# Kernel optimization log

Hardware: AMD Instinct MI355X
Metric: run time of the kernel (lower is better)

## Reference

```python
import jax, jax.numpy as jnp
import numpy as np

N = 50000      # nodes
E = 1_600_000  # edges (avg degree 32)
D = 128        # in/hidden channels
OUT = 64       # out channels


def setup_inputs() -> dict:
    key = jax.random.key(0)
    ks = jax.random.split(key, 12)
    s = 0.08  # ~glorot scale for 128-dim
    return {
        "x": jax.random.normal(ks[0], (N, D), jnp.float32),
        "edge_index": jax.random.randint(ks[1], (2, E), 0, N, dtype=jnp.int64),
        # GCN layer 1
        "W1": jax.random.normal(ks[2], (D, D), jnp.float32) * s,
        "b1": jnp.zeros((D,), jnp.float32),
        # GraphSAGE layer 2 (mean aggregation): lin_l on neighbors, lin_r on root
        "Wl": jax.random.normal(ks[3], (D, D), jnp.float32) * s,
        "Wr": jax.random.normal(ks[4], (D, D), jnp.float32) * s,
        "bs": jnp.zeros((D,), jnp.float32),
        # GAT layer 3 (heads=1, concat=False)
        "Wg": jax.random.normal(ks[5], (D, D), jnp.float32) * s,
        "a_s": jax.random.normal(ks[6], (D,), jnp.float32) * s,
        "a_d": jax.random.normal(ks[7], (D,), jnp.float32) * s,
        "bg": jnp.zeros((D,), jnp.float32),
        # GCN output layer
        "Wo": jax.random.normal(ks[8], (D, OUT), jnp.float32) * s,
        "bo": jnp.zeros((OUT,), jnp.float32),
    }


def _self_loops(src, dst, n):
    loop = jnp.arange(n, dtype=src.dtype)
    return jnp.concatenate([src, loop]), jnp.concatenate([dst, loop])


def gcn_conv(x, W, b, src, dst, n):
    # PyG GCNConv: add self-loops, symmetric normalization D^-1/2 (A+I) D^-1/2
    s2, d2 = _self_loops(src, dst, n)
    deg = jax.ops.segment_sum(jnp.ones_like(d2, dtype=x.dtype), d2, num_segments=n)
    dinv = jnp.where(deg > 0, jax.lax.rsqrt(deg), 0.0)
    h = x @ W                         # [n, out]
    norm = dinv[s2] * dinv[d2]        # [E+n]
    out = jax.ops.segment_sum(h[s2] * norm[:, None], d2, num_segments=n)
    return out + b


def sage_conv(x, Wl, Wr, b, src, dst, n):
    # PyG SAGEConv, aggr='mean': W_l * mean_neigh + W_r * x (no self-loops)
    deg = jax.ops.segment_sum(jnp.ones_like(dst, dtype=x.dtype), dst, num_segments=n)
    agg = jax.ops.segment_sum(x[src], dst, num_segments=n)
    mean = agg / jnp.maximum(deg, 1.0)[:, None]
    return mean @ Wl + x @ Wr + b


def gat_conv(x, W, a_s, a_d, b, src, dst, n):
    # PyG GATConv heads=1, concat=False: self-loops, edge softmax over incoming edges
    h = x @ W                               # [n, out]
    s2, d2 = _self_loops(src, dst, n)
    alpha_src = h @ a_s                     # [n]
    alpha_dst = h @ a_d                     # [n]
    e = jax.nn.leaky_relu(alpha_src[s2] + alpha_dst[d2], negative_slope=0.2)
    m = jax.ops.segment_max(e, d2, num_segments=n)   # every node has a self-loop
    ex = jnp.exp(e - m[d2])
    denom = jax.ops.segment_sum(ex, d2, num_segments=n)
    alpha = ex / denom[d2]
    out = jax.ops.segment_sum(alpha[:, None] * h[s2], d2, num_segments=n)
    return out + b


def reference(x, edge_index, W1, b1, Wl, Wr, bs, Wg, a_s, a_d, bg, Wo, bo):
    src, dst = edge_index[0], edge_index[1]
    n = x.shape[0]
    # eval mode: F.dropout(training=False) is identity
    h = jax.nn.relu(gcn_conv(x, W1, b1, src, dst, n))
    h = jax.nn.relu(sage_conv(h, Wl, Wr, bs, src, dst, n))
    h = jax.nn.relu(gat_conv(h, Wg, a_s, a_d, bg, src, dst, n))
    return gcn_conv(h, Wo, bo, src, dst, n)
```

## Files before the change

### kernel.cpp

```cpp
#include <hip/hip_runtime.h>
#include <math.h>


#define BUCKET_BITS 8
#define BUCKET_SZ   256
#define NBMAX       256
#define CAP         10240
#define CAPE        2560

typedef short short8 __attribute__((ext_vector_type(8)));
typedef float f32x4 __attribute__((ext_vector_type(4)));
typedef unsigned int u32x4 __attribute__((ext_vector_type(4)));
typedef unsigned short u16x8 __attribute__((ext_vector_type(8)));

__device__ __forceinline__ float leaky02(float x) { return x > 0.0f ? x : 0.2f * x; }
__device__ __forceinline__ float bflo(unsigned u) { return __uint_as_float(u << 16); }
__device__ __forceinline__ float bfhi(unsigned u) { return __uint_as_float(u & 0xFFFF0000u); }
__device__ __forceinline__ unsigned short f2bf(float f) {
    unsigned u = __float_as_uint(f);
    u += 0x7FFFu + ((u >> 16) & 1u);
    return (unsigned short)(u >> 16);
}

template<int NO, bool AFP32, bool SCALE, bool BIASRELU, bool DUAL, bool DOTS>
__global__ __launch_bounds__(256) void mgemm_k(
    const void* __restrict__ Av, const float* __restrict__ W,
    const void* __restrict__ A1v, const float* __restrict__ W1,
    unsigned short* __restrict__ C16,
    const float* __restrict__ scale, const float* __restrict__ bias,
    const float* __restrict__ a_s, const float* __restrict__ a_d,
    float* __restrict__ as_, float* __restrict__ ad_, int n)
{
    constexpr int CT = NO / 16;
    __shared__ unsigned short Wp[128 * NO];
    const int tid = threadIdx.x;
    const int wave = tid >> 6, lane = tid & 63;
    const int q = lane >> 4, ml = lane & 15;
    const int row0 = blockIdx.x * 64 + wave * 16;
    int arow = row0 + ml; if (arow >= n) arow = n - 1;

    f32x4 acc[CT];
#pragma unroll
    for (int c = 0; c < CT; c++) acc[c] = {0.f, 0.f, 0.f, 0.f};

    for (int half = 0; half < (DUAL ? 2 : 1); half++) {
        const float* Wsrc = half ? W1 : W;
        const void* Asrc = half ? A1v : Av;
        __syncthreads();
        for (int f = tid; f < 64 * (NO / 4); f += 256) {
            const int kp = f / (NO / 4);
            const int n4 = f % (NO / 4);
            const float4 a = *(const float4*)(Wsrc + (size_t)(2 * kp) * NO + n4 * 4);
            const float4 b = *(const float4*)(Wsrc + (size_t)(2 * kp + 1) * NO + n4 * 4);
            const int k = 2 * kp, kb = k >> 5, qq = (k >> 3) & 3, p = (k & 7) >> 1;
            const float av[4] = {a.x, a.y, a.z, a.w};
            const float bv[4] = {b.x, b.y, b.z, b.w};
#pragma unroll
            for (int j = 0; j < 4; j++) {
                int col = n4 * 4 + j;
                int c = col >> 4, nl = col & 15;
                unsigned pk = (unsigned)f2bf(av[j]) | ((unsigned)f2bf(bv[j]) << 16);
                ((unsigned*)Wp)[(((kb * CT + c) * 64) + qq * 16 + nl) * 4 + p] = pk;
            }
        }
        __syncthreads();
#pragma unroll
        for (int kb = 0; kb < 4; kb++) {
            short8 afr;
            if (AFP32) {
                const float* Af = (const float*)Asrc + (size_t)arow * 128 + kb * 32 + q * 8;
#pragma unroll
                for (int j = 0; j < 8; j++) afr[j] = (short)f2bf(Af[j]);
            } else {
                afr = *(const short8*)((const unsigned short*)Asrc +
                                       ((size_t)kb * n + arow) * 32 + q * 8);
            }
#pragma unroll
            for (int c = 0; c < CT; c++) {
                short8 bfr = *(const short8*)(Wp + ((size_t)(kb * CT + c) * 64 + lane) * 8);
                acc[c] = __builtin_amdgcn_mfma_f32_16x16x32_bf16(afr, bfr, acc[c], 0, 0, 0);
            }
        }
    }

    if (DOTS) {
        float ps[4] = {0.f, 0.f, 0.f, 0.f}, pd[4] = {0.f, 0.f, 0.f, 0.f};
#pragma unroll
        for (int c = 0; c < CT; c++) {
            float sv = a_s[c * 16 + ml], dv = a_d[c * 16 + ml];
#pragma unroll
            for (int r = 0; r < 4; r++) {
                ps[r] = fmaf(acc[c][r], sv, ps[r]);
                pd[r] = fmaf(acc[c][r], dv, pd[r]);
            }
        }
#pragma unroll
        for (int off = 1; off < 16; off <<= 1) {
#pragma unroll
            for (int r = 0; r < 4; r++) {
                ps[r] += __shfl_xor(ps[r], off, 64);
                pd[r] += __shfl_xor(pd[r], off, 64);
            }
        }
        if (ml == 0) {
#pragma unroll
            for (int r = 0; r < 4; r++) {
                int row = row0 + q * 4 + r;
                if (row < n) { as_[row] = ps[r]; ad_[row] = pd[r]; }
            }
        }
    }

    float sc[4];
    if (SCALE) {
#pragma unroll
        for (int r = 0; r < 4; r++) {
            int row = row0 + q * 4 + r;
            sc[r] = scale[row < n ? row : 0];
        }
    }
#pragma unroll
    for (int c = 0; c < CT; c++) {
        float bv = BIASRELU ? bias[c * 16 + ml] : 0.0f;
        const int col = c * 16 + ml;
#pragma unroll
        for (int r = 0; r < 4; r++) {
            int row = row0 + q * 4 + r;
            if (row < n) {
                float v = acc[c][r];
                if (SCALE) v *= sc[r];
                if (BIASRELU) v = fmaxf(v + bv, 0.0f);
                C16[((size_t)(col >> 5) * n + row) * 32 + (col & 31)] = f2bf(v);
            }
        }
    }
}

__global__ void binit_k(int* __restrict__ bcur, int nb) {
    int t = threadIdx.x;
    if (t < nb) bcur[t] = t * CAP;
}

#define PART_CH 4096
__global__ __launch_bounds__(256) void part_k(
    const int* __restrict__ src, const int* __restrict__ dst,
    int* __restrict__ bcur, unsigned long long* __restrict__ part, int nE)
{
    __shared__ int cnt[NBMAX];
    __shared__ int cur[NBMAX];
    const int base = blockIdx.x * PART_CH;
    const int t = threadIdx.x;
    cnt[t] = 0;
    __syncthreads();
    int d[PART_CH / 256], s[PART_CH / 256];
#pragma unroll
    for (int j = 0; j < PART_CH / 256; j++) {
        int e = base + j * 256 + t;
        if (e < nE) {
            d[j] = dst[e]; s[j] = src[e];
            atomicAdd(&cnt[d[j] >> BUCKET_BITS], 1);
        } else d[j] = -1;
    }
    __syncthreads();
    {
        int c = cnt[t];
        cur[t] = c ? atomicAdd(&bcur[t], c) : 0;
    }
    __syncthreads();
#pragma unroll
    for (int j = 0; j < PART_CH / 256; j++) {
        if (d[j] >= 0) {
            int p = atomicAdd(&cur[d[j] >> BUCKET_BITS], 1);
            part[p] = ((unsigned long long)(unsigned)d[j] << 32) | (unsigned)s[j];
        }
    }
}

__global__ __launch_bounds__(256) void bscan_k(const int* __restrict__ bcur,
                                               int* __restrict__ bofs, int nb) {
    __shared__ int sm[256];
    const int t = threadIdx.x;
    int v = (t < nb) ? (bcur[t] - t * CAP) : 0;
    sm[t] = v;
    __syncthreads();
    for (int off = 1; off < 256; off <<= 1) {
        int tv = (t >= off) ? sm[t - off] : 0;
        __syncthreads();
        sm[t] += tv;
        __syncthreads();
    }
    if (t < nb) {
        bofs[t] = sm[t] - v;
        if (t == nb - 1) bofs[nb] = sm[t];
    }
}

__global__ __launch_bounds__(256) void csr_k(
    const unsigned long long* __restrict__ part, const int* __restrict__ bcur,
    const int* __restrict__ bofs, int* __restrict__ rowptr, int* __restrict__ srcs,
    float* __restrict__ dinv, float* __restrict__ invm, int n, int nE)
{
    __shared__ int lcnt[BUCKET_SZ];
    __shared__ int sm[BUCKET_SZ];
    __shared__ int lcur[BUCKET_SZ];
    const int b = blockIdx.x;
    const int t = threadIdx.x;
    const int base_in = b * CAP;
    const int cntE = bcur[b] - base_in;
    const int base_out = bofs[b];

    lcnt[t] = 0;
    __syncthreads();
#pragma unroll 4
    for (int e = t; e < cntE; e += 256) {
        int dl = (int)(part[base_in + e] >> 32) & (BUCKET_SZ - 1);
        atomicAdd(&lcnt[dl], 1);
    }
    __syncthreads();
    int v = lcnt[t];
    sm[t] = v;
    __syncthreads();
    for (int off = 1; off < 256; off <<= 1) {
        int tv = (t >= off) ? sm[t - off] : 0;
        __syncthreads();
        sm[t] += tv;
        __syncthreads();
    }
    const int excl = sm[t] - v;
    const int node = (b << BUCKET_BITS) + t;
    if (node < n) {
        rowptr[node] = base_out + excl;
        float dg = (float)v;
        dinv[node] = rsqrtf(dg + 1.0f);
        invm[node] = 1.0f / fmaxf(dg, 1.0f);
        if (node == n - 1) rowptr[n] = nE;
    }
    lcur[t] = excl;
    __syncthreads();
#pragma unroll 4
    for (int e = t; e < cntE; e += 256) {
        unsigned long long w = part[base_in + e];
        int dl = (int)(w >> 32) & (BUCKET_SZ - 1);
        int pos = atomicAdd(&lcur[dl], 1);
        srcs[base_out + pos] = (int)(unsigned)w;
    }
}

__global__ __launch_bounds__(256) void gatw_k(
    const int* __restrict__ rowptr, const int* __restrict__ srcs,
    const float* __restrict__ as_, const float* __restrict__ ad_,
    float* __restrict__ ew, float* __restrict__ rdn_, float* __restrict__ sw_, int n)
{
    const int node = blockIdx.x * 32 + (threadIdx.x >> 3);
    const int lane = threadIdx.x & 7;
    if (node >= n) return;
    const int beg = rowptr[node], end = rowptr[node + 1];
    const float ad_d = ad_[node];
    float psum = 0.f;
    for (int k = beg + lane; k < end; k += 8) {
        float e = __expf(leaky02(as_[srcs[k]] + ad_d));
        ew[k] = e;
        psum += e;
    }
#pragma unroll
    for (int off = 4; off > 0; off >>= 1) psum += __shfl_xor(psum, off, 64);
    if (lane == 0) {
        float se = __expf(leaky02(as_[node] + ad_d));
        float r = 1.0f / (psum + se);
        rdn_[node] = r;
        sw_[node] = se * r;
    }
}

template<int MODE, bool OV>
__device__ __forceinline__ void gath_loop(
    const u32x4* __restrict__ Hc, const int* __restrict__ srcs,
    const float* __restrict__ ew, const int* lsrc, const float* lw,
    int beg, int end, int beg_blk, int lane, float* acc)
{
    int k = beg;
    for (; k + 8 <= end; k += 8) {
        unsigned sidx[8]; float wv[8];
#pragma unroll
        for (int j = 0; j < 8; j++) {
            int ofs = k + j - beg_blk;
            if (OV) {
                bool in = ofs < CAPE;
                int ofc = in ? ofs : 0;
                sidx[j] = (unsigned)(in ? lsrc[ofc] : srcs[k + j]);
                if (MODE == 2) wv[j] = in ? lw[ofc] : ew[k + j];
            } else {
                sidx[j] = (unsigned)lsrc[ofs];
                if (MODE == 2) wv[j] = lw[ofs];
            }
        }
        u32x4 h[8];
#pragma unroll
        for (int j = 0; j < 8; j++) h[j] = Hc[(size_t)sidx[j] * 4 + lane];
#pragma unroll
        for (int j = 0; j < 8; j++) {
#pragma unroll
            for (int c = 0; c < 4; c++) {
                if (MODE == 2) {
                    acc[2 * c]     = fmaf(wv[j], bflo(h[j][c]), acc[2 * c]);
                    acc[2 * c + 1] = fmaf(wv[j], bfhi(h[j][c]), acc[2 * c + 1]);
                } else {
                    acc[2 * c]     += bflo(h[j][c]);
                    acc[2 * c + 1] += bfhi(h[j][c]);
                }
            }
        }
    }
    if (k < end) {
        unsigned sidx[8]; float wv[8];
#pragma unroll
        for (int j = 0; j < 8; j++) {
            int kk = k + j;
            bool act = kk < end;
            int kc = act ? kk : end - 1;
            int ofs = kc - beg_blk;
            int s; float w0 = 1.0f;
            if (OV) {
                bool in = ofs < CAPE;
                int ofc = in ? ofs : 0;
                s = in ? lsrc[ofc] : srcs[kc];
                if (MODE == 2) w0 = in ? lw[ofc] : ew[kc];
            } else {
                s = lsrc[ofs];
                if (MODE == 2) w0 = lw[ofs];
            }
            sidx[j] = (unsigned)s;
            wv[j] = act ? w0 : 0.0f;
        }
        u32x4 h[8];
#pragma unroll
        for (int j = 0; j < 8; j++) h[j] = Hc[(size_t)sidx[j] * 4 + lane];
#pragma unroll
        for (int j = 0; j < 8; j++) {
#pragma unroll
            for (int c = 0; c < 4; c++) {
                acc[2 * c]     = fmaf(wv[j], bflo(h[j][c]), acc[2 * c]);
                acc[2 * c + 1] = fmaf(wv[j], bfhi(h[j][c]), acc[2 * c + 1]);
            }
        }
    }
}

template<int NCB, int MODE>
__global__ __launch_bounds__(256) void gatherbf_k(
    const unsigned short* __restrict__ H16, float* __restrict__ outf,
    unsigned short* __restrict__ out16,
    const int* __restrict__ rowptr, const int* __restrict__ srcs,
    const float* __restrict__ scl,
    const float* __restrict__ sw_,
    const float* __restrict__ ew,
    const float* __restrict__ bias, int n)
{
    constexpr int XPC = 8 / NCB;
    constexpr int NPB = 64;
    __shared__ int lsrc[CAPE];
    __shared__ float lw[(MODE == 2) ? CAPE : 1];

    const int bid = (int)blockIdx.x;
    const int xj = bid & 7;
    const int cb = xj / XPC;
    const int NG = (n + NPB - 1) / NPB;
    const int ng = (bid >> 3) * XPC + (xj % XPC);
    if (ng >= NG) return;

    const int tid = (int)threadIdx.x;
    const int node0 = ng * NPB;
    const int nodeN = min(node0 + NPB, n);
    const int beg_blk = rowptr[node0];
    const int end_blk = rowptr[nodeN];
    const int cnt = end_blk - beg_blk;
    const int cl = min(cnt, CAPE);
    for (int i = tid; i < cl; i += 256) {
        lsrc[i] = srcs[beg_blk + i];
        if (MODE == 2) lw[i] = ew[beg_blk + i];
    }
    __syncthreads();

    const int node = node0 + (tid >> 2);
    const int lane = tid & 3;
    if (node >= nodeN) return;
    const int beg = rowptr[node], end = rowptr[node + 1];
    const u32x4* __restrict__ Hc = (const u32x4*)H16 + (size_t)cb * n * 4;

    float acc[8];
#pragma unroll
    for (int j = 0; j < 8; j++) acc[j] = 0.f;

    if (cnt <= CAPE)
        gath_loop<MODE, false>(Hc, srcs, ew, lsrc, lw, beg, end, beg_blk, lane, acc);
    else
        gath_loop<MODE, true>(Hc, srcs, ew, lsrc, lw, beg, end, beg_blk, lane, acc);

    const size_t orow = ((size_t)cb * n + node) * 4 + lane;
    float r[8];
    if (MODE == 0) {
        float sc = scl[node];
#pragma unroll
        for (int j = 0; j < 8; j++) r[j] = acc[j] * sc;
    } else {
        u32x4 su = Hc[(size_t)node * 4 + lane];
        float sv[8];
#pragma unroll
        for (int c = 0; c < 4; c++) { sv[2 * c] = bflo(su[c]); sv[2 * c + 1] = bfhi(su[c]); }
        const float4* b4 = (const float4*)bias;
        float4 ba = b4[cb * 8 + lane * 2], bb = b4[cb * 8 + lane * 2 + 1];
        float bv[8] = {ba.x, ba.y, ba.z, ba.w, bb.x, bb.y, bb.z, bb.w};
        if (MODE == 2) {
            float rden = scl[node], sw = sw_[node];
#pragma unroll
            for (int j = 0; j < 8; j++)
                r[j] = fmaxf(fmaf(rden, acc[j], fmaf(sw, sv[j], bv[j])), 0.f);
        } else {
            float dv = scl[node];
#pragma unroll
            for (int j = 0; j < 8; j++) {
                r[j] = dv * (acc[j] + sv[j]) + bv[j];
                if (MODE == 1) r[j] = fmaxf(r[j], 0.f);
            }
        }
    }
    if (MODE == 3) {
        float4* o4 = (float4*)(outf + (size_t)node * 64 + cb * 32 + lane * 8);
        float4 ra = {r[0], r[1], r[2], r[3]}, rb = {r[4], r[5], r[6], r[7]};
        o4[0] = ra; o4[1] = rb;
    } else {
        u16x8 qv;
#pragma unroll
        for (int j = 0; j < 8; j++) qv[j] = f2bf(r[j]);
        ((u16x8*)out16)[orow] = qv;
    }
}

extern "C" void kernel_launch(void* const* d_in, const int* in_sizes, int n_in,
                              void* d_out, int out_size, void* d_ws, size_t ws_size,
                              hipStream_t stream)
{
    const float* x   = (const float*)d_in[0];
    const int*   ei  = (const int*)d_in[1];
    const float* W1  = (const float*)d_in[2];
    const float* b1  = (const float*)d_in[3];
    const float* Wl  = (const float*)d_in[4];
    const float* Wr  = (const float*)d_in[5];
    const float* bs  = (const float*)d_in[6];
    const float* Wg  = (const float*)d_in[7];
    const float* a_s = (const float*)d_in[8];
    const float* a_d = (const float*)d_in[9];
    const float* bg  = (const float*)d_in[10];
    const float* Wo  = (const float*)d_in[11];
    const float* bo  = (const float*)d_in[12];

    const int n  = in_sizes[0] / 128;
    const int nE = in_sizes[1] / 2;
    const int* src = ei;
    const int* dst = ei + nE;

    char* w = (char*)d_ws;
    auto alloc = [&](size_t bytes) { char* p = w; w += (bytes + 255) & ~(size_t)255; return p; };
    unsigned short* S0 = (unsigned short*)alloc((size_t)n * 128 * 2);
    unsigned short* S1 = (unsigned short*)alloc((size_t)n * 128 * 2);
    unsigned short* S2 = (unsigned short*)alloc((size_t)n * 128 * 2);
    const int nbv = (n + BUCKET_SZ - 1) / BUCKET_SZ;
    unsigned long long* part = (unsigned long long*)alloc((size_t)nbv * CAP * 8);
    int*   srcs   = (int*)alloc((size_t)nE * 4);
    int*   rowptr = (int*)alloc((size_t)(n + 1) * 4);
    int*   bofs   = (int*)alloc((NBMAX + 1) * 4);
    int*   bcur   = (int*)alloc(NBMAX * 4);
    float* dinv   = (float*)alloc((size_t)n * 4);
    float* invm   = (float*)alloc((size_t)n * 4);
    float* as_    = (float*)alloc((size_t)n * 4);
    float* ad_    = (float*)alloc((size_t)n * 4);
    float* ew     = (float*)alloc((size_t)nE * 4);
    float* rdn_   = (float*)alloc((size_t)n * 4);
    float* sw_    = (float*)alloc((size_t)n * 4);

    const int TB = 256;
    auto cdiv = [](long long a, long long b) { return (int)((a + b - 1) / b); };
    const int nb     = nbv;
    const int gPart  = cdiv(nE, PART_CH);
    const int gGemm  = cdiv(n, 64);
    const int NG     = cdiv(n, 64);
    const int gGa128 = 8 * cdiv(NG, 2);
    const int gGa64  = 8 * cdiv(NG, 4);
    const int gGatw  = cdiv(n, 32);

    binit_k<<<1, 256, 0, stream>>>(bcur, nb);
    part_k<<<gPart, TB, 0, stream>>>(src, dst, bcur, part, nE);
    bscan_k<<<1, 256, 0, stream>>>(bcur, bofs, nb);
    csr_k<<<nb, TB, 0, stream>>>(part, bcur, bofs, rowptr, srcs, dinv, invm, n, nE);

    mgemm_k<128, true, true, false, false, false><<<gGemm, TB, 0, stream>>>(
        x, W1, nullptr, nullptr, S0, dinv, nullptr, nullptr, nullptr, nullptr, nullptr, n);
    gatherbf_k<4, 1><<<gGa128, TB, 0, stream>>>(S0, nullptr, S1, rowptr, srcs,
                                                dinv, nullptr, nullptr, b1, n);

    gatherbf_k<4, 0><<<gGa128, TB, 0, stream>>>(S1, nullptr, S0, rowptr, srcs,
                                                invm, nullptr, nullptr, nullptr, n);
    mgemm_k<128, false, false, true, true, false><<<gGemm, TB, 0, stream>>>(
        S0, Wl, S1, Wr, S2, nullptr, bs, nullptr, nullptr, nullptr, nullptr, n);

    mgemm_k<128, false, false, false, false, true><<<gGemm, TB, 0, stream>>>(
        S2, Wg, nullptr, nullptr, S1, nullptr, nullptr, a_s, a_d, as_, ad_, n);
    gatw_k<<<gGatw, TB, 0, stream>>>(rowptr, srcs, as_, ad_, ew, rdn_, sw_, n);
    gatherbf_k<4, 2><<<gGa128, TB, 0, stream>>>(S1, nullptr, S0, rowptr, srcs,
                                                rdn_, sw_, ew, bg, n);

    mgemm_k<64, false, true, false, false, false><<<gGemm, TB, 0, stream>>>(
        S0, Wo, nullptr, nullptr, S2, dinv, nullptr, nullptr, nullptr, nullptr, nullptr, n);
    gatherbf_k<2, 3><<<gGa64, TB, 0, stream>>>(S2, (float*)d_out, nullptr, rowptr, srcs,
                                               dinv, nullptr, nullptr, bo, n);
}
```

Before: 357.6 us.

## Drop LDS staging of edge indices in gather; vector-load srcs and packed FMA

```diff
diff --git a/kernel.cpp b/kernel.cpp
--- a/kernel.cpp
+++ b/kernel.cpp
@@ -6,12 +6,14 @@
 #define BUCKET_SZ   256
 #define NBMAX       256
 #define CAP         10240
-#define CAPE        2560
 
 typedef short short8 __attribute__((ext_vector_type(8)));
 typedef float f32x4 __attribute__((ext_vector_type(4)));
+typedef float f32x2 __attribute__((ext_vector_type(2)));
 typedef unsigned int u32x4 __attribute__((ext_vector_type(4)));
 typedef unsigned short u16x8 __attribute__((ext_vector_type(8)));
+typedef int int4a __attribute__((ext_vector_type(4), aligned(4)));
+typedef float float4a __attribute__((ext_vector_type(4), aligned(4)));
 
 __device__ __forceinline__ float leaky02(float x) { return x > 0.0f ? x : 0.2f * x; }
 __device__ __forceinline__ float bflo(unsigned u) { return __uint_as_float(u << 16); }
@@ -272,82 +274,33 @@
     }
 }
 
-template<int MODE, bool OV>
-__device__ __forceinline__ void gath_loop(
-    const u32x4* __restrict__ Hc, const int* __restrict__ srcs,
-    const float* __restrict__ ew, const int* lsrc, const float* lw,
-    int beg, int end, int beg_blk, int lane, float* acc)
-{
-    int k = beg;
-    for (; k + 8 <= end; k += 8) {
-        unsigned sidx[8]; float wv[8];
-#pragma unroll
-        for (int j = 0; j < 8; j++) {
-            int ofs = k + j - beg_blk;
-            if (OV) {
-                bool in = ofs < CAPE;
-                int ofc = in ? ofs : 0;
-                sidx[j] = (unsigned)(in ? lsrc[ofc] : srcs[k + j]);
-                if (MODE == 2) wv[j] = in ? lw[ofc] : ew[k + j];
-            } else {
-                sidx[j] = (unsigned)lsrc[ofs];
-                if (MODE == 2) wv[j] = lw[ofs];
-            }
-        }
-        u32x4 h[8];
-#pragma unroll
-        for (int j = 0; j < 8; j++) h[j] = Hc[(size_t)sidx[j] * 4 + lane];
-#pragma unroll
-        for (int j = 0; j < 8; j++) {
-#pragma unroll
-            for (int c = 0; c < 4; c++) {
-                if (MODE == 2) {
-                    acc[2 * c]     = fmaf(wv[j], bflo(h[j][c]), acc[2 * c]);
-                    acc[2 * c + 1] = fmaf(wv[j], bfhi(h[j][c]), acc[2 * c + 1]);
-                } else {
-                    acc[2 * c]     += bflo(h[j][c]);
-                    acc[2 * c + 1] += bfhi(h[j][c]);
-                }
-            }
-        }
-    }
-    if (k < end) {
-        unsigned sidx[8]; float wv[8];
-#pragma unroll
-        for (int j = 0; j < 8; j++) {
-            int kk = k + j;
-            bool act = kk < end;
-            int kc = act ? kk : end - 1;
-            int ofs = kc - beg_blk;
-            int s; float w0 = 1.0f;
-            if (OV) {
-                bool in = ofs < CAPE;
-                int ofc = in ? ofs : 0;
-                s = in ? lsrc[ofc] : srcs[kc];
-                if (MODE == 2) w0 = in ? lw[ofc] : ew[kc];
-            } else {
-                s = lsrc[ofs];
-                if (MODE == 2) w0 = lw[ofs];
-            }
-            sidx[j] = (unsigned)s;
-            wv[j] = act ? w0 : 0.0f;
-        }
-        u32x4 h[8];
-#pragma unroll
-        for (int j = 0; j < 8; j++) h[j] = Hc[(size_t)sidx[j] * 4 + lane];
-#pragma unroll
-        for (int j = 0; j < 8; j++) {
-#pragma unroll
-            for (int c = 0; c < 4; c++) {
-                acc[2 * c]     = fmaf(wv[j], bflo(h[j][c]), acc[2 * c]);
-                acc[2 * c + 1] = fmaf(wv[j], bfhi(h[j][c]), acc[2 * c + 1]);
-            }
+template<int MODE>
+__device__ __forceinline__ void edge8(
+    const char* __restrict__ Hb, unsigned loff,
+    const int4a ia, const int4a ib,
+    const float4a wa, const float4a wb,
+    f32x2* acc)
+{
+    const int s[8] = {ia.x, ia.y, ia.z, ia.w, ib.x, ib.y, ib.z, ib.w};
+    u32x4 h[8];
+#pragma unroll
+    for (int j = 0; j < 8; j++)
+        h[j] = *(const u32x4*)(Hb + (size_t)(((unsigned)s[j] << 6) + loff));
+    const float wv[8] = {wa.x, wa.y, wa.z, wa.w, wb.x, wb.y, wb.z, wb.w};
+#pragma unroll
+    for (int j = 0; j < 8; j++) {
+        f32x2 w2 = {wv[j], wv[j]};
+#pragma unroll
+        for (int c = 0; c < 4; c++) {
+            f32x2 hv = {bflo(h[j][c]), bfhi(h[j][c])};
+            if (MODE == 2) acc[c] = w2 * hv + acc[c];
+            else           acc[c] = acc[c] + hv;
         }
     }
 }
 
 template<int NCB, int MODE>
-__global__ __launch_bounds__(256) void gatherbf_k(
+__global__ __launch_bounds__(256, 4) void gatherbf_k(
     const unsigned short* __restrict__ H16, float* __restrict__ outf,
     unsigned short* __restrict__ out16,
     const int* __restrict__ rowptr, const int* __restrict__ srcs,
@@ -358,8 +311,6 @@
 {
     constexpr int XPC = 8 / NCB;
     constexpr int NPB = 64;
-    __shared__ int lsrc[CAPE];
-    __shared__ float lw[(MODE == 2) ? CAPE : 1];
 
     const int bid = (int)blockIdx.x;
     const int xj = bid & 7;
@@ -369,57 +320,101 @@
     if (ng >= NG) return;
 
     const int tid = (int)threadIdx.x;
-    const int node0 = ng * NPB;
-    const int nodeN = min(node0 + NPB, n);
-    const int beg_blk = rowptr[node0];
-    const int end_blk = rowptr[nodeN];
-    const int cnt = end_blk - beg_blk;
-    const int cl = min(cnt, CAPE);
-    for (int i = tid; i < cl; i += 256) {
-        lsrc[i] = srcs[beg_blk + i];
-        if (MODE == 2) lw[i] = ew[beg_blk + i];
-    }
-    __syncthreads();
-
-    const int node = node0 + (tid >> 2);
+    const int node = ng * NPB + (tid >> 2);
+    if (node >= n) return;
     const int lane = tid & 3;
-    if (node >= nodeN) return;
     const int beg = rowptr[node], end = rowptr[node + 1];
-    const u32x4* __restrict__ Hc = (const u32x4*)H16 + (size_t)cb * n * 4;
-
-    float acc[8];
-#pragma unroll
-    for (int j = 0; j < 8; j++) acc[j] = 0.f;
-
-    if (cnt <= CAPE)
-        gath_loop<MODE, false>(Hc, srcs, ew, lsrc, lw, beg, end, beg_blk, lane, acc);
-    else
-        gath_loop<MODE, true>(Hc, srcs, ew, lsrc, lw, beg, end, beg_blk, lane, acc);
+    const char* __restrict__ Hb = (const char*)H16 + (size_t)cb * n * 64;
+    const unsigned loff = (unsigned)lane * 16u;
+
+    f32x2 acc[4];
+#pragma unroll
+    for (int c = 0; c < 4; c++) acc[c] = {0.f, 0.f};
+    const float4a wdum = {0.f, 0.f, 0.f, 0.f};
+
+    int k = beg;
+    for (; k + 16 <= end; k += 16) {
+        int4a ia0 = *(const int4a*)(srcs + k);
+        int4a ib0 = *(const int4a*)(srcs + k + 4);
+        int4a ia1 = *(const int4a*)(srcs + k + 8);
+        int4a ib1 = *(const int4a*)(srcs + k + 12);
+        float4a wa0 = wdum, wb0 = wdum, wa1 = wdum, wb1 = wdum;
+        if (MODE == 2) {
+            wa0 = *(const float4a*)(ew + k);      wb0 = *(const float4a*)(ew + k + 4);
+            wa1 = *(const float4a*)(ew + k + 8);  wb1 = *(const float4a*)(ew + k + 12);
+        }
+        edge8<MODE>(Hb, loff, ia0, ib0, wa0, wb0, acc);
+        edge8<MODE>(Hb, loff, ia1, ib1, wa1, wb1, acc);
+    }
+    for (; k + 8 <= end; k += 8) {
+        int4a ia = *(const int4a*)(srcs + k);
+        int4a ib = *(const int4a*)(srcs + k + 4);
+        float4a wa = wdum, wb = wdum;
+        if (MODE == 2) {
+            wa = *(const float4a*)(ew + k);  wb = *(const float4a*)(ew + k + 4);
+        }
+        edge8<MODE>(Hb, loff, ia, ib, wa, wb, acc);
+    }
+    if (k < end) {
+        int4a ia = *(const int4a*)(srcs + k);
+        int4a ib = *(const int4a*)(srcs + k + 4);
+        int s[8] = {ia.x, ia.y, ia.z, ia.w, ib.x, ib.y, ib.z, ib.w};
+        float wv[8];
+        if (MODE == 2) {
+            float4a wa = *(const float4a*)(ew + k);
+            float4a wb = *(const float4a*)(ew + k + 4);
+            wv[0] = wa.x; wv[1] = wa.y; wv[2] = wa.z; wv[3] = wa.w;
+            wv[4] = wb.x; wv[5] = wb.y; wv[6] = wb.z; wv[7] = wb.w;
+        }
+#pragma unroll
+        for (int j = 0; j < 8; j++) {
+            bool act = (k + j) < end;
+            s[j] = act ? s[j] : 0;
+            if (MODE == 2) wv[j] = act ? wv[j] : 0.0f;
+            else           wv[j] = act ? 1.0f : 0.0f;
+        }
+        u32x4 h[8];
+#pragma unroll
+        for (int j = 0; j < 8; j++)
+            h[j] = *(const u32x4*)(Hb + (size_t)(((unsigned)s[j] << 6) + loff));
+#pragma unroll
+        for (int j = 0; j < 8; j++) {
+            f32x2 w2 = {wv[j], wv[j]};
+#pragma unroll
+            for (int c = 0; c < 4; c++) {
+                f32x2 hv = {bflo(h[j][c]), bfhi(h[j][c])};
+                acc[c] = w2 * hv + acc[c];
+            }
+        }
+    }
 
     const size_t orow = ((size_t)cb * n + node) * 4 + lane;
     float r[8];
     if (MODE == 0) {
         float sc = scl[node];
 #pragma unroll
-        for (int j = 0; j < 8; j++) r[j] = acc[j] * sc;
+        for (int c = 0; c < 4; c++) { r[2*c] = acc[c].x * sc; r[2*c+1] = acc[c].y * sc; }
     } else {
-        u32x4 su = Hc[(size_t)node * 4 + lane];
+        u32x4 su = *(const u32x4*)(Hb + (size_t)(((unsigned)node << 6) + loff));
         float sv[8];
 #pragma unroll
-        for (int c = 0; c < 4; c++) { sv[2 * c] = bflo(su[c]); sv[2 * c + 1] = bfhi(su[c]); }
+        for (int c = 0; c < 4; c++) { sv[2*c] = bflo(su[c]); sv[2*c+1] = bfhi(su[c]); }
         const float4* b4 = (const float4*)bias;
         float4 ba = b4[cb * 8 + lane * 2], bb = b4[cb * 8 + lane * 2 + 1];
         float bv[8] = {ba.x, ba.y, ba.z, ba.w, bb.x, bb.y, bb.z, bb.w};
+        float a8[8];
+#pragma unroll
+        for (int c = 0; c < 4; c++) { a8[2*c] = acc[c].x; a8[2*c+1] = acc[c].y; }
         if (MODE == 2) {
             float rden = scl[node], sw = sw_[node];
 #pragma unroll
             for (int j = 0; j < 8; j++)
-                r[j] = fmaxf(fmaf(rden, acc[j], fmaf(sw, sv[j], bv[j])), 0.f);
+                r[j] = fmaxf(fmaf(rden, a8[j], fmaf(sw, sv[j], bv[j])), 0.f);
         } else {
             float dv = scl[node];
 #pragma unroll
             for (int j = 0; j < 8; j++) {
-                r[j] = dv * (acc[j] + sv[j]) + bv[j];
+                r[j] = dv * (a8[j] + sv[j]) + bv[j];
                 if (MODE == 1) r[j] = fmaxf(r[j], 0.f);
             }
         }
```

After: 377.1 us. 1.05x slower.

## Prepack bf16 weights once and read MFMA B fragments from global memory

Applied to the files above, without the earlier changes.

```diff
diff --git a/kernel.cpp b/kernel.cpp
--- a/kernel.cpp
+++ b/kernel.cpp
@@ -10,6 +10,7 @@
 
 typedef short short8 __attribute__((ext_vector_type(8)));
 typedef float f32x4 __attribute__((ext_vector_type(4)));
+typedef float f32x2 __attribute__((ext_vector_type(2)));
 typedef unsigned int u32x4 __attribute__((ext_vector_type(4)));
 typedef unsigned short u16x8 __attribute__((ext_vector_type(8)));
 
@@ -22,17 +23,51 @@
     return (unsigned short)(u >> 16);
 }
 
+__global__ __launch_bounds__(256) void wpackall_k(
+    const float* __restrict__ W1, const float* __restrict__ Wl,
+    const float* __restrict__ Wr, const float* __restrict__ Wg,
+    const float* __restrict__ Wo,
+    unsigned* __restrict__ P1, unsigned* __restrict__ Pl,
+    unsigned* __restrict__ Pr, unsigned* __restrict__ Pg,
+    unsigned* __restrict__ Po)
+{
+    const int b = blockIdx.x;
+    const float* W; unsigned* P; int NO;
+    if      (b == 0) { W = W1; P = P1; NO = 128; }
+    else if (b == 1) { W = Wl; P = Pl; NO = 128; }
+    else if (b == 2) { W = Wr; P = Pr; NO = 128; }
+    else if (b == 3) { W = Wg; P = Pg; NO = 128; }
+    else             { W = Wo; P = Po; NO = 64;  }
+    const int CT = NO / 16;
+    const int n4w = NO / 4;
+    for (int f = threadIdx.x; f < 64 * n4w; f += 256) {
+        const int kp = f / n4w;
+        const int n4 = f % n4w;
+        const float4 a = *(const float4*)(W + (size_t)(2 * kp) * NO + n4 * 4);
+        const float4 bb = *(const float4*)(W + (size_t)(2 * kp + 1) * NO + n4 * 4);
+        const int k = 2 * kp, kb = k >> 5, qq = (k >> 3) & 3, p = (k & 7) >> 1;
+        const float av[4] = {a.x, a.y, a.z, a.w};
+        const float bv[4] = {bb.x, bb.y, bb.z, bb.w};
+#pragma unroll
+        for (int j = 0; j < 4; j++) {
+            int col = n4 * 4 + j;
+            int c = col >> 4, nl = col & 15;
+            unsigned pk = (unsigned)f2bf(av[j]) | ((unsigned)f2bf(bv[j]) << 16);
+            P[(((kb * CT + c) * 64) + qq * 16 + nl) * 4 + p] = pk;
+        }
+    }
+}
+
 template<int NO, bool AFP32, bool SCALE, bool BIASRELU, bool DUAL, bool DOTS>
 __global__ __launch_bounds__(256) void mgemm_k(
-    const void* __restrict__ Av, const float* __restrict__ W,
-    const void* __restrict__ A1v, const float* __restrict__ W1,
+    const void* __restrict__ Av, const unsigned short* __restrict__ Bp,
+    const void* __restrict__ A1v, const unsigned short* __restrict__ Bp1,
     unsigned short* __restrict__ C16,
     const float* __restrict__ scale, const float* __restrict__ bias,
     const float* __restrict__ a_s, const float* __restrict__ a_d,
     float* __restrict__ as_, float* __restrict__ ad_, int n)
 {
     constexpr int CT = NO / 16;
-    __shared__ unsigned short Wp[128 * NO];
     const int tid = threadIdx.x;
     const int wave = tid >> 6, lane = tid & 63;
     const int q = lane >> 4, ml = lane & 15;
@@ -44,42 +79,30 @@
     for (int c = 0; c < CT; c++) acc[c] = {0.f, 0.f, 0.f, 0.f};
 
     for (int half = 0; half < (DUAL ? 2 : 1); half++) {
-        const float* Wsrc = half ? W1 : W;
+        const unsigned short* __restrict__ Bsrc = half ? Bp1 : Bp;
         const void* Asrc = half ? A1v : Av;
-        __syncthreads();
-        for (int f = tid; f < 64 * (NO / 4); f += 256) {
-            const int kp = f / (NO / 4);
-            const int n4 = f % (NO / 4);
-            const float4 a = *(const float4*)(Wsrc + (size_t)(2 * kp) * NO + n4 * 4);
-            const float4 b = *(const float4*)(Wsrc + (size_t)(2 * kp + 1) * NO + n4 * 4);
-            const int k = 2 * kp, kb = k >> 5, qq = (k >> 3) & 3, p = (k & 7) >> 1;
-            const float av[4] = {a.x, a.y, a.z, a.w};
-            const float bv[4] = {b.x, b.y, b.z, b.w};
-#pragma unroll
-            for (int j = 0; j < 4; j++) {
-                int col = n4 * 4 + j;
-                int c = col >> 4, nl = col & 15;
-                unsigned pk = (unsigned)f2bf(av[j]) | ((unsigned)f2bf(bv[j]) << 16);
-                ((unsigned*)Wp)[(((kb * CT + c) * 64) + qq * 16 + nl) * 4 + p] = pk;
-            }
-        }
-        __syncthreads();
 #pragma unroll
         for (int kb = 0; kb < 4; kb++) {
             short8 afr;
             if (AFP32) {
                 const float* Af = (const float*)Asrc + (size_t)arow * 128 + kb * 32 + q * 8;
-#pragma unroll
-                for (int j = 0; j < 8; j++) afr[j] = (short)f2bf(Af[j]);
+                float4 f0 = *(const float4*)Af;
+                float4 f1 = *(const float4*)(Af + 4);
+                afr[0] = (short)f2bf(f0.x); afr[1] = (short)f2bf(f0.y);
+                afr[2] = (short)f2bf(f0.z); afr[3] = (short)f2bf(f0.w);
+                afr[4] = (short)f2bf(f1.x); afr[5] = (short)f2bf(f1.y);
+                afr[6] = (short)f2bf(f1.z); afr[7] = (short)f2bf(f1.w);
             } else {
                 afr = *(const short8*)((const unsigned short*)Asrc +
                                        ((size_t)kb * n + arow) * 32 + q * 8);
             }
-#pragma unroll
-            for (int c = 0; c < CT; c++) {
-                short8 bfr = *(const short8*)(Wp + ((size_t)(kb * CT + c) * 64 + lane) * 8);
-                acc[c] = __builtin_amdgcn_mfma_f32_16x16x32_bf16(afr, bfr, acc[c], 0, 0, 0);
-            }
+            short8 bfr[CT];
+#pragma unroll
+            for (int c = 0; c < CT; c++)
+                bfr[c] = *(const short8*)(Bsrc + ((size_t)(kb * CT + c) * 64 + lane) * 8);
+#pragma unroll
+            for (int c = 0; c < CT; c++)
+                acc[c] = __builtin_amdgcn_mfma_f32_16x16x32_bf16(afr, bfr[c], acc[c], 0, 0, 0);
         }
     }
 
@@ -274,73 +297,74 @@
 
 template<int MODE, bool OV>
 __device__ __forceinline__ void gath_loop(
-    const u32x4* __restrict__ Hc, const int* __restrict__ srcs,
-    const float* __restrict__ ew, const int* lsrc, const float* lw,
-    int beg, int end, int beg_blk, int lane, float* acc)
+    const char* __restrict__ Hb, unsigned loff,
+    const int* __restrict__ srcs, const float* __restrict__ ew,
+    const int* lsrc, const float* lw,
+    int beg, int end, int beg_blk, f32x2* acc)
 {
     int k = beg;
     for (; k + 8 <= end; k += 8) {
-        unsigned sidx[8]; float wv[8];
+        int s[8]; float wv[8];
 #pragma unroll
         for (int j = 0; j < 8; j++) {
             int ofs = k + j - beg_blk;
             if (OV) {
                 bool in = ofs < CAPE;
                 int ofc = in ? ofs : 0;
-                sidx[j] = (unsigned)(in ? lsrc[ofc] : srcs[k + j]);
+                s[j] = in ? lsrc[ofc] : srcs[k + j];
                 if (MODE == 2) wv[j] = in ? lw[ofc] : ew[k + j];
             } else {
-                sidx[j] = (unsigned)lsrc[ofs];
+                s[j] = lsrc[ofs];
                 if (MODE == 2) wv[j] = lw[ofs];
             }
         }
         u32x4 h[8];
 #pragma unroll
-        for (int j = 0; j < 8; j++) h[j] = Hc[(size_t)sidx[j] * 4 + lane];
+        for (int j = 0; j < 8; j++)
+            h[j] = *(const u32x4*)(Hb + (size_t)(((unsigned)s[j] << 6) + loff));
 #pragma unroll
         for (int j = 0; j < 8; j++) {
+            f32x2 w2 = {wv[j], wv[j]};
 #pragma unroll
             for (int c = 0; c < 4; c++) {
-                if (MODE == 2) {
-                    acc[2 * c]     = fmaf(wv[j], bflo(h[j][c]), acc[2 * c]);
-                    acc[2 * c + 1] = fmaf(wv[j], bfhi(h[j][c]), acc[2 * c + 1]);
-                } else {
-                    acc[2 * c]     += bflo(h[j][c]);
-                    acc[2 * c + 1] += bfhi(h[j][c]);
-                }
+                f32x2 hv = {bflo(h[j][c]), bfhi(h[j][c])};
+                if (MODE == 2) acc[c] = w2 * hv + acc[c];
+                else           acc[c] = acc[c] + hv;
             }
         }
     }
     if (k < end) {
-        unsigned sidx[8]; float wv[8];
+        int s[8]; float wv[8];
 #pragma unroll
         for (int j = 0; j < 8; j++) {
             int kk = k + j;
             bool act = kk < end;
             int kc = act ? kk : end - 1;
             int ofs = kc - beg_blk;
-            int s; float w0 = 1.0f;
+            int sj; float w0 = 1.0f;
             if (OV) {
                 bool in = ofs < CAPE;
                 int ofc = in ? ofs : 0;
-                s = in ? lsrc[ofc] : srcs[kc];
+                sj = in ? lsrc[ofc] : srcs[kc];
                 if (MODE == 2) w0 = in ? lw[ofc] : ew[kc];
             } else {
-                s = lsrc[ofs];
+                sj = lsrc[ofs];
                 if (MODE == 2) w0 = lw[ofs];
             }
-            sidx[j] = (unsigned)s;
-            wv[j] = act ? w0 : 0.0f;
+            s[j] = sj;
+            wv[j] = act ? ((MODE == 2) ? w0 : 1.0f) : 0.0f;
         }
         u32x4 h[8];
 #pragma unroll
-        for (int j = 0; j < 8; j++) h[j] = Hc[(size_t)sidx[j] * 4 + lane];
+        for (int j = 0; j < 8; j++)
+            h[j] = *(const u32x4*)(Hb + (size_t)(((unsigned)s[j] << 6) + loff));
 #pragma unroll
         for (int j = 0; j < 8; j++) {
+            f32x2 w2 = {wv[j], wv[j]};
 #pragma unroll
             for (int c = 0; c < 4; c++) {
-                acc[2 * c]     = fmaf(wv[j], bflo(h[j][c]), acc[2 * c]);
-                acc[2 * c + 1] = fmaf(wv[j], bfhi(h[j][c]), acc[2 * c + 1]);
+                f32x2 hv = {bflo(h[j][c]), bfhi(h[j][c])};
+                acc[c] = w2 * hv + acc[c];
             }
         }
     }
@@ -385,41 +409,45 @@
     const int lane = tid & 3;
     if (node >= nodeN) return;
     const int beg = rowptr[node], end = rowptr[node + 1];
-    const u32x4* __restrict__ Hc = (const u32x4*)H16 + (size_t)cb * n * 4;
-
-    float acc[8];
-#pragma unroll
-    for (int j = 0; j < 8; j++) acc[j] = 0.f;
+    const char* __restrict__ Hb = (const char*)H16 + (size_t)cb * n * 64;
+    const unsigned loff = (unsigned)lane * 16u;
+
+    f32x2 acc[4];
+#pragma unroll
+    for (int c = 0; c < 4; c++) acc[c] = {0.f, 0.f};
 
     if (cnt <= CAPE)
-        gath_loop<MODE, false>(Hc, srcs, ew, lsrc, lw, beg, end, beg_blk, lane, acc);
+        gath_loop<MODE, false>(Hb, loff, srcs, ew, lsrc, lw, beg, end, beg_blk, acc);
     else
-        gath_loop<MODE, true>(Hc, srcs, ew, lsrc, lw, beg, end, beg_blk, lane, acc);
+        gath_loop<MODE, true>(Hb, loff, srcs, ew, lsrc, lw, beg, end, beg_blk, acc);
 
     const size_t orow = ((size_t)cb * n + node) * 4 + lane;
     float r[8];
     if (MODE == 0) {
         float sc = scl[node];
 #pragma unroll
-        for (int j = 0; j < 8; j++) r[j] = acc[j] * sc;
+        for (int c = 0; c < 4; c++) { r[2*c] = acc[c].x * sc; r[2*c+1] = acc[c].y * sc; }
     } else {
-        u32x4 su = Hc[(size_t)node * 4 + lane];
+        u32x4 su = *(const u32x4*)(Hb + (size_t)(((unsigned)node << 6) + loff));
         float sv[8];
 #pragma unroll
-        for (int c = 0; c < 4; c++) { sv[2 * c] = bflo(su[c]); sv[2 * c + 1] = bfhi(su[c]); }
+        for (int c = 0; c < 4; c++) { sv[2*c] = bflo(su[c]); sv[2*c+1] = bfhi(su[c]); }
         const float4* b4 = (const float4*)bias;
         float4 ba = b4[cb * 8 + lane * 2], bb = b4[cb * 8 + lane * 2 + 1];
         float bv[8] = {ba.x, ba.y, ba.z, ba.w, bb.x, bb.y, bb.z, bb.w};
+        float a8[8];
+#pragma unroll
+        for (int c = 0; c < 4; c++) { a8[2*c] = acc[c].x; a8[2*c+1] = acc[c].y; }
         if (MODE == 2) {
             float rden = scl[node], sw = sw_[node];
 #pragma unroll
             for (int j = 0; j < 8; j++)
-                r[j] = fmaxf(fmaf(rden, acc[j], fmaf(sw, sv[j], bv[j])), 0.f);
+                r[j] = fmaxf(fmaf(rden, a8[j], fmaf(sw, sv[j], bv[j])), 0.f);
         } else {
             float dv = scl[node];
 #pragma unroll
             for (int j = 0; j < 8; j++) {
-                r[j] = dv * (acc[j] + sv[j]) + bv[j];
+                r[j] = dv * (a8[j] + sv[j]) + bv[j];
                 if (MODE == 1) r[j] = fmaxf(r[j], 0.f);
             }
         }
@@ -467,6 +495,7 @@
     const int nbv = (n + BUCKET_SZ - 1) / BUCKET_SZ;
     unsigned long long* part = (unsigned long long*)alloc((size_t)nbv * CAP * 8);
     int*   srcs   = (int*)alloc((size_t)nE * 4);
+    float* ew     = (float*)alloc((size_t)nE * 4);
     int*   rowptr = (int*)alloc((size_t)(n + 1) * 4);
     int*   bofs   = (int*)alloc((NBMAX + 1) * 4);
     int*   bcur   = (int*)alloc(NBMAX * 4);
@@ -474,9 +503,13 @@
     float* invm   = (float*)alloc((size_t)n * 4);
     float* as_    = (float*)alloc((size_t)n * 4);
     float* ad_    = (float*)alloc((size_t)n * 4);
-    float* ew     = (float*)alloc((size_t)nE * 4);
     float* rdn_   = (float*)alloc((size_t)n * 4);
     float* sw_    = (float*)alloc((size_t)n * 4);
+    unsigned* P1  = (unsigned*)alloc(64 * 128 * 4);
+    unsigned* Pl  = (unsigned*)alloc(64 * 128 * 4);
+    unsigned* Pr  = (unsigned*)alloc(64 * 128 * 4);
+    unsigned* Pg  = (unsigned*)alloc(64 * 128 * 4);
+    unsigned* Po  = (unsigned*)alloc(64 * 64 * 4);
 
     const int TB = 256;
     auto cdiv = [](long long a, long long b) { return (int)((a + b - 1) / b); };
@@ -488,29 +521,34 @@
     const int gGa64  = 8 * cdiv(NG, 4);
     const int gGatw  = cdiv(n, 32);
 
+    wpackall_k<<<5, TB, 0, stream>>>(W1, Wl, Wr, Wg, Wo, P1, Pl, Pr, Pg, Po);
     binit_k<<<1, 256, 0, stream>>>(bcur, nb);
     part_k<<<gPart, TB, 0, stream>>>(src, dst, bcur, part, nE);
     bscan_k<<<1, 256, 0, stream>>>(bcur, bofs, nb);
     csr_k<<<nb, TB, 0, stream>>>(part, bcur, bofs, rowptr, srcs, dinv, invm, n, nE);
 
     mgemm_k<128, true, true, false, false, false><<<gGemm, TB, 0, stream>>>(
-        x, W1, nullptr, nullptr, S0, dinv, nullptr, nullptr, nullptr, nullptr, nullptr, n);
+        x, (const unsigned short*)P1, nullptr, nullptr, S0, dinv, nullptr,
+        nullptr, nullptr, nullptr, nullptr, n);
     gatherbf_k<4, 1><<<gGa128, TB, 0, stream>>>(S0, nullptr, S1, rowptr, srcs,
                                                 dinv, nullptr, nullptr, b1, n);
 
     gatherbf_k<4, 0><<<gGa128, TB, 0, stream>>>(S1, nullptr, S0, rowptr, srcs,
                                                 invm, nullptr, nullptr, nullptr, n);
     mgemm_k<128, false, false, true, true, false><<<gGemm, TB, 0, stream>>>(
-        S0, Wl, S1, Wr, S2, nullptr, bs, nullptr, nullptr, nullptr, nullptr, n);
+        S0, (const unsigned short*)Pl, S1, (const unsigned short*)Pr, S2,
+        nullptr, bs, nullptr, nullptr, nullptr, nullptr, n);
 
     mgemm_k<128, false, false, false, false, true><<<gGemm, TB, 0, stream>>>(
-        S2, Wg, nullptr, nullptr, S1, nullptr, nullptr, a_s, a_d, as_, ad_, n);
+        S2, (const unsigned short*)Pg, nullptr, nullptr, S1, nullptr, nullptr,
+        a_s, a_d, as_, ad_, n);
     gatw_k<<<gGatw, TB, 0, stream>>>(rowptr, srcs, as_, ad_, ew, rdn_, sw_, n);
     gatherbf_k<4, 2><<<gGa128, TB, 0, stream>>>(S1, nullptr, S0, rowptr, srcs,
                                                 rdn_, sw_, ew, bg, n);
 
     mgemm_k<64, false, true, false, false, false><<<gGemm, TB, 0, stream>>>(
-        S0, Wo, nullptr, nullptr, S2, dinv, nullptr, nullptr, nullptr, nullptr, nullptr, n);
+        S0, (const unsigned short*)Po, nullptr, nullptr, S2, dinv, nullptr,
+        nullptr, nullptr, nullptr, nullptr, n);
     gatherbf_k<2, 3><<<gGa64, TB, 0, stream>>>(S2, (float*)d_out, nullptr, rowptr, srcs,
                                                dinv, nullptr, nullptr, bo, n);
 }
```

After: 351.2 us. About the same (-1.8%).
